# Kernel tuning notes

Hardware: AMD Instinct MI355X
Metric: run time of the kernel (lower is better)

## Reference

```python
import jax, jax.numpy as jnp
import numpy as np

NEG_INF = -1.0e9


def setup_inputs() -> dict:
    key = jax.random.key(0)
    k1, k2, k3, k4 = jax.random.split(key, 4)
    B, N, F, U, H = 4, 2048, 128, 64, 4
    x = jax.random.normal(k1, (B, N, F), dtype=jnp.float32)
    adj = jax.random.randint(k2, (B, N, N), 0, 2, dtype=jnp.int32)
    W = jax.random.normal(k3, (H, F, U), dtype=jnp.float32) * (1.0 / np.sqrt(F))
    b = jnp.zeros((H, U), dtype=jnp.float32)
    a_w = jax.random.normal(k4, (H, U), dtype=jnp.float32) * (1.0 / np.sqrt(U))
    a_b = jnp.zeros((H,), dtype=jnp.float32)
    return {"x": x, "adj": adj, "W": W, "b": b, "a_w": a_w, "a_b": a_b}


def reference(x, adj, W, b, a_w, a_b):
    # Per-head Dense + relu, batched over heads: proj [H,B,N,U]
    proj = jax.nn.relu(jnp.einsum('bnf,hfu->hbnu', x, W) + b[:, None, None, :])
    # Scalar attention score per node: s [H,B,N]
    s = jnp.einsum('hbnu,hu->hbn', proj, a_w) + a_b[:, None, None]
    # Outer-product logits [H,B,N,N], masked by adjacency
    logits = s[:, :, :, None] * s[:, :, None, :]
    logits = jnp.where(adj[None] > 0, logits, NEG_INF)
    scores = jax.nn.softmax(logits, axis=-1)
    # Weighted aggregation, then mean over heads -> [B,N,U]
    out = jnp.einsum('hbij,hbju->hbiu', scores, proj)
    return jnp.mean(out, axis=0)
```

## Files before the change

### kernel.cpp

```cpp
#include <hip/hip_runtime.h>
#include <hip/hip_bf16.h>


#define Bdim 4
#define Ndim 2048
#define Fdim 128
#define Udim 64
#define Hdim 4
#define JC 2
#define JCHUNK (Ndim / JC)

typedef __attribute__((ext_vector_type(8))) short short8;
typedef __attribute__((ext_vector_type(4))) float f32x4;

__device__ __forceinline__ void splitbf(float f, short& hi, short& lo) {
  union { __hip_bfloat16 b; unsigned short u; } ch, cl;
  ch.b = __float2bfloat16(f);
  cl.b = __float2bfloat16(f - __bfloat162float(ch.b));
  hi = (short)ch.u;
  lo = (short)cl.u;
}

__device__ __forceinline__ void stage16(const void* g, void* l) {
  __builtin_amdgcn_global_load_lds(
      (const __attribute__((address_space(1))) unsigned int*)g,
      (__attribute__((address_space(3))) unsigned int*)l, 16, 0, 0);
}

__global__ __launch_bounds__(256) void pack_adj_kernel(
    const int* __restrict__ adj, unsigned long long* __restrict__ bits,
    int nchunks) {
  const int lane = threadIdx.x & 63;
  const int wid = (blockIdx.x * 256 + threadIdx.x) >> 6;
  const int nw = (gridDim.x * 256) >> 6;
  for (int c = wid * 4; c + 3 < nchunks; c += nw * 4) {
    int v0 = adj[(size_t)(c + 0) * 64 + lane];
    int v1 = adj[(size_t)(c + 1) * 64 + lane];
    int v2 = adj[(size_t)(c + 2) * 64 + lane];
    int v3 = adj[(size_t)(c + 3) * 64 + lane];
    unsigned long long m0 = __ballot(v0 != 0);
    unsigned long long m1 = __ballot(v1 != 0);
    unsigned long long m2 = __ballot(v2 != 0);
    unsigned long long m3 = __ballot(v3 != 0);
    if (lane == 0) {
      bits[c + 0] = m0;
      bits[c + 1] = m1;
      bits[c + 2] = m2;
      bits[c + 3] = m3;
    }
  }
}

__global__ __launch_bounds__(256) void proj_kernel(
    const float* __restrict__ x, const float* __restrict__ W,
    const float* __restrict__ bias, const float* __restrict__ a_w,
    const float* __restrict__ a_b, unsigned short* __restrict__ pTh,
    unsigned short* __restrict__ pTl, float* __restrict__ s) {
  const int bid = blockIdx.x;
  const int nt = bid & 31;
  const int b = (bid >> 5) & 3;
  const int h = bid >> 7;
  const int n0 = nt * 64;

  __shared__ __align__(16) char smem[71168];
  float (*Wl)[Udim] = (float(*)[Udim])(smem);
  float (*xl)[Fdim + 4] = (float(*)[Fdim + 4])(smem + 32768);
  float (*pt)[68] = (float(*)[68])(smem + 32768);
  float* bl = (float*)(smem + 66560);
  float* awl = (float*)(smem + 66816);
  float (*sred)[16] = (float(*)[16])(smem + 67072);

  const int t = threadIdx.x;

  const float* Wg = W + (size_t)h * Fdim * Udim;
  for (int k = t; k < Fdim * Udim / 4; k += 256) {
    ((float4*)&Wl[0][0])[k] = ((const float4*)Wg)[k];
  }
  if (t < Udim) {
    bl[t] = bias[h * Udim + t];
    awl[t] = a_w[h * Udim + t];
  }
  const float* xg = x + ((size_t)b * Ndim + n0) * Fdim;
  for (int k = t; k < 64 * Fdim / 4; k += 256) {
    int row = k >> 5;
    int c4 = k & 31;
    float4 v = ((const float4*)xg)[(size_t)row * (Fdim / 4) + c4];
    *(float4*)&xl[row][c4 * 4] = v;
  }
  __syncthreads();

  const int ug = t & 15, rg = t >> 4;
  const int u0 = ug * 4, r0 = rg * 4;
  float acc[4][4] = {};

#pragma unroll 4
  for (int f = 0; f < Fdim; ++f) {
    const float4 wv = *(const float4*)&Wl[f][u0];
    const float xv[4] = {xl[r0][f], xl[r0 + 1][f], xl[r0 + 2][f], xl[r0 + 3][f]};
#pragma unroll
    for (int c = 0; c < 4; ++c) {
      acc[c][0] = fmaf(xv[c], wv.x, acc[c][0]);
      acc[c][1] = fmaf(xv[c], wv.y, acc[c][1]);
      acc[c][2] = fmaf(xv[c], wv.z, acc[c][2]);
      acc[c][3] = fmaf(xv[c], wv.w, acc[c][3]);
    }
  }

  float po[4][4];
#pragma unroll
  for (int c = 0; c < 4; ++c)
#pragma unroll
    for (int k = 0; k < 4; ++k)
      po[c][k] = fmaxf(acc[c][k] + bl[u0 + k], 0.f);

#pragma unroll
  for (int c = 0; c < 4; ++c) {
    float sp = po[c][0] * awl[u0 + 0] + po[c][1] * awl[u0 + 1] +
               po[c][2] * awl[u0 + 2] + po[c][3] * awl[u0 + 3];
    sred[r0 + c][ug] = sp;
  }
  __syncthreads();

#pragma unroll
  for (int k = 0; k < 4; ++k) {
    float4 v = {po[0][k], po[1][k], po[2][k], po[3][k]};
    *(float4*)&pt[u0 + k][r0] = v;
  }
  __syncthreads();

  const size_t hb = (size_t)h * Bdim + b;
  const int su = t >> 2;
  const int snl = (t & 3) * 16;
  float v[16];
#pragma unroll
  for (int j = 0; j < 4; ++j)
    *(float4*)&v[4 * j] = *(const float4*)&pt[su][snl + 4 * j];
  short hi[16], lo[16];
#pragma unroll
  for (int k = 0; k < 16; ++k) splitbf(v[k], hi[k], lo[k]);
  unsigned short* ph =
      pTh + hb * (size_t)(Udim * Ndim) + (size_t)su * Ndim + n0 + snl;
  unsigned short* pl =
      pTl + hb * (size_t)(Udim * Ndim) + (size_t)su * Ndim + n0 + snl;
  *(short8*)(ph + 0) = *(short8*)&hi[0];
  *(short8*)(ph + 8) = *(short8*)&hi[8];
  *(short8*)(pl + 0) = *(short8*)&lo[0];
  *(short8*)(pl + 8) = *(short8*)&lo[8];

  if (t < 64) {
    float sum = a_b[h];
#pragma unroll
    for (int k = 0; k < 16; ++k) sum += sred[t][k];
    s[hb * Ndim + n0 + t] = sum;
  }
}

__global__ __launch_bounds__(256, 4) void attn_mfma_kernel(
    const unsigned short* __restrict__ pTh,
    const unsigned short* __restrict__ pTl, const float* __restrict__ s,
    const unsigned int* __restrict__ abits, float* __restrict__ out_part,
    float* __restrict__ Z_part) {
  const int bid = blockIdx.x;
  const int jc = bid & 1;
  const int it = (bid >> 1) & 31;
  const int b = (bid >> 6) & 3;
  const int h = bid >> 8;
  const int i0g = it * 64;
  const int j0g = jc * JCHUNK;

  __shared__ float sj[JCHUNK];
  __shared__ unsigned int ab[64][33];
  __shared__ short Bst[2][8][512];
  __shared__ float zl[4][4][16];

  const int t = threadIdx.x;
  const int wv = t >> 6;
  const int lane = t & 63;
  const int q = lane >> 4;
  const int li = lane & 15;
  const size_t hb = (size_t)h * Bdim + b;
  const float* sg = s + hb * Ndim;

  ((float4*)sj)[t] = ((const float4*)(sg + j0g))[t];
  for (int k = t; k < 64 * 32; k += 256) {
    int row = k >> 5, w = k & 31;
    ab[row][w] =
        abits[((size_t)b * Ndim + i0g + row) * (Ndim / 32) + (j0g >> 5) + w];
  }
  const int irow = wv * 16 + li;

  const unsigned short* bsrc_h =
      pTh + hb * (size_t)(Udim * Ndim) + (size_t)(wv * 16 + li) * Ndim + j0g +
      q * 8;
  const unsigned short* bsrc_l =
      pTl + hb * (size_t)(Udim * Ndim) + (size_t)(wv * 16 + li) * Ndim + j0g +
      q * 8;

  stage16(bsrc_h, &Bst[0][wv * 2 + 0][0]);
  stage16(bsrc_l, &Bst[0][wv * 2 + 1][0]);

  f32x4 acc[4] = {};
  float zacc = 0.f;
  __syncthreads();

  const float si = sg[i0g + irow];
  int buf = 0;

  for (int js = 0; js < JCHUNK; js += 32) {
    if (js + 32 < JCHUNK) {
      stage16(bsrc_h + js + 32, &Bst[buf ^ 1][wv * 2 + 0][0]);
      stage16(bsrc_l + js + 32, &Bst[buf ^ 1][wv * 2 + 1][0]);
    }
    const short8 b0h = *(const short8*)&Bst[buf][0][lane * 8];
    const short8 b0l = *(const short8*)&Bst[buf][1][lane * 8];
    const short8 b1h = *(const short8*)&Bst[buf][2][lane * 8];
    const short8 b1l = *(const short8*)&Bst[buf][3][lane * 8];
    const short8 b2h = *(const short8*)&Bst[buf][4][lane * 8];
    const short8 b2l = *(const short8*)&Bst[buf][5][lane * 8];
    const short8 b3h = *(const short8*)&Bst[buf][6][lane * 8];
    const short8 b3l = *(const short8*)&Bst[buf][7][lane * 8];
    const unsigned int mb = (ab[irow][js >> 5] >> (q * 8)) & 0xffu;
    const f32x4 s0 = *(const f32x4*)&sj[js + q * 8];
    const f32x4 s1 = *(const f32x4*)&sj[js + q * 8 + 4];
    const float sv[8] = {s0.x, s0.y, s0.z, s0.w, s1.x, s1.y, s1.z, s1.w};
    short8 ahi, alo;
#pragma unroll
    for (int e = 0; e < 8; ++e) {
      float we = __expf(si * sv[e]);
      we = ((mb >> e) & 1u) ? we : 0.f;
      zacc += we;
      short hh, ll;
      splitbf(we, hh, ll);
      ahi[e] = hh;
      alo[e] = ll;
    }
    acc[0] = __builtin_amdgcn_mfma_f32_16x16x32_bf16(ahi, b0h, acc[0], 0, 0, 0);
    acc[1] = __builtin_amdgcn_mfma_f32_16x16x32_bf16(ahi, b1h, acc[1], 0, 0, 0);
    acc[2] = __builtin_amdgcn_mfma_f32_16x16x32_bf16(ahi, b2h, acc[2], 0, 0, 0);
    acc[3] = __builtin_amdgcn_mfma_f32_16x16x32_bf16(ahi, b3h, acc[3], 0, 0, 0);
    acc[0] = __builtin_amdgcn_mfma_f32_16x16x32_bf16(alo, b0h, acc[0], 0, 0, 0);
    acc[1] = __builtin_amdgcn_mfma_f32_16x16x32_bf16(alo, b1h, acc[1], 0, 0, 0);
    acc[2] = __builtin_amdgcn_mfma_f32_16x16x32_bf16(alo, b2h, acc[2], 0, 0, 0);
    acc[3] = __builtin_amdgcn_mfma_f32_16x16x32_bf16(alo, b3h, acc[3], 0, 0, 0);
    acc[0] = __builtin_amdgcn_mfma_f32_16x16x32_bf16(ahi, b0l, acc[0], 0, 0, 0);
    acc[1] = __builtin_amdgcn_mfma_f32_16x16x32_bf16(ahi, b1l, acc[1], 0, 0, 0);
    acc[2] = __builtin_amdgcn_mfma_f32_16x16x32_bf16(ahi, b2l, acc[2], 0, 0, 0);
    acc[3] = __builtin_amdgcn_mfma_f32_16x16x32_bf16(ahi, b3l, acc[3], 0, 0, 0);
    __syncthreads();
    buf ^= 1;
  }

  zl[wv][q][li] = zacc;
  __syncthreads();

  const size_t pslab = ((size_t)h * JC + jc) * Bdim + b;
  if (q == 0) {
    float z = zl[wv][0][li] + zl[wv][1][li] + zl[wv][2][li] + zl[wv][3][li];
    Z_part[pslab * Ndim + i0g + wv * 16 + li] = z;
  }
  float* op = out_part + (pslab * Ndim + i0g + wv * 16) * Udim;
#pragma unroll
  for (int r = 0; r < 4; ++r) {
    const int ir = q * 4 + r;
#pragma unroll
    for (int m = 0; m < 4; ++m) {
      op[(size_t)ir * Udim + m * 16 + li] = acc[m][r];
    }
  }
}

__global__ __launch_bounds__(256) void combine_kernel(
    const float* __restrict__ out_part, const float* __restrict__ Z_part,
    float* __restrict__ out) {
  const int idx = blockIdx.x * 256 + threadIdx.x;
  const int u4 = idx & 15;
  const size_t bn = (size_t)(idx >> 4);
  float4 r = {0.f, 0.f, 0.f, 0.f};
#pragma unroll
  for (int h = 0; h < Hdim; ++h) {
    const size_t s0 = ((size_t)h * JC + 0) * (Bdim * Ndim) + bn;
    const size_t s1 = ((size_t)h * JC + 1) * (Bdim * Ndim) + bn;
    float4 p0 = ((const float4*)out_part)[s0 * (Udim / 4) + u4];
    float4 p1 = ((const float4*)out_part)[s1 * (Udim / 4) + u4];
    float z = Z_part[s0] + Z_part[s1];
    z = (z != 0.f) ? z : 1.f;
    const float inv = 1.f / z;
    r.x += (p0.x + p1.x) * inv;
    r.y += (p0.y + p1.y) * inv;
    r.z += (p0.z + p1.z) * inv;
    r.w += (p0.w + p1.w) * inv;
  }
  r.x *= 0.25f; r.y *= 0.25f; r.z *= 0.25f; r.w *= 0.25f;
  ((float4*)out)[idx] = r;
}

extern "C" void kernel_launch(void* const* d_in, const int* in_sizes, int n_in,
                              void* d_out, int out_size, void* d_ws,
                              size_t ws_size, hipStream_t stream) {
  const float* x = (const float*)d_in[0];
  const int* adj = (const int*)d_in[1];
  const float* W = (const float*)d_in[2];
  const float* bias = (const float*)d_in[3];
  const float* a_w = (const float*)d_in[4];
  const float* a_b = (const float*)d_in[5];
  float* out = (float*)d_out;

  char* ws = (char*)d_ws;
  unsigned short* pTh = (unsigned short*)(ws + 0);
  unsigned short* pTl = (unsigned short*)(ws + 4194304);
  float* s = (float*)(ws + 8388608);
  unsigned int* adjbits = (unsigned int*)(ws + 8519680);
  float* out_part = (float*)(ws + 10616832);
  float* Z_part = (float*)(ws + 27394048);

  const int nchunks = Bdim * Ndim * Ndim / 64;
  pack_adj_kernel<<<2048, 256, 0, stream>>>(adj, (unsigned long long*)adjbits,
                                            nchunks);
  proj_kernel<<<Hdim * Bdim * 32, 256, 0, stream>>>(x, W, bias, a_w, a_b, pTh,
                                                    pTl, s);
  attn_mfma_kernel<<<Hdim * Bdim * 32 * JC, 256, 0, stream>>>(
      pTh, pTl, s, adjbits, out_part, Z_part);
  combine_kernel<<<(Bdim * Ndim * Udim / 4) / 256, 256, 0, stream>>>(
      out_part, Z_part, out);
}
```

Before: 166.4 us.

## Split attention over four j-chunks, stage output through LDS, shuffle-reduce Z

Doubles the number of j-column chunks per attention block, so there are twice as many blocks, each with half the work and a smaller shared-memory footprint, and raises the occupancy hint to 7 blocks. The Z partial sums are now reduced with wave shuffles instead of LDS, and accumulator output goes through a transposed LDS buffer so global stores are float4 and coalesced. The hi/lo bf16 split now truncates for the high part. The costs are more partial-output traffic and a combine kernel that sums four chunks instead of two.

```diff
diff --git a/kernel.cpp b/kernel.cpp
--- a/kernel.cpp
+++ b/kernel.cpp
@@ -7,18 +7,23 @@
 #define Fdim 128
 #define Udim 64
 #define Hdim 4
-#define JC 2
+#define JC 4
 #define JCHUNK (Ndim / JC)
 
 typedef __attribute__((ext_vector_type(8))) short short8;
 typedef __attribute__((ext_vector_type(4))) float f32x4;
 
+__device__ __forceinline__ short bf16_rne(float f) {
+  union { __hip_bfloat16 b; unsigned short u; } c;
+  c.b = __float2bfloat16(f);
+  return (short)c.u;
+}
+
 __device__ __forceinline__ void splitbf(float f, short& hi, short& lo) {
-  union { __hip_bfloat16 b; unsigned short u; } ch, cl;
-  ch.b = __float2bfloat16(f);
-  cl.b = __float2bfloat16(f - __bfloat162float(ch.b));
-  hi = (short)ch.u;
-  lo = (short)cl.u;
+  unsigned u = __float_as_uint(f);
+  hi = (short)(u >> 16);
+  float lof = f - __uint_as_float(u & 0xffff0000u);
+  lo = bf16_rne(lof);
 }
 
 __device__ __forceinline__ void stage16(const void* g, void* l) {
@@ -155,23 +160,22 @@
   }
 }
 
-__global__ __launch_bounds__(256, 4) void attn_mfma_kernel(
+__global__ __launch_bounds__(256, 7) void attn_mfma_kernel(
     const unsigned short* __restrict__ pTh,
     const unsigned short* __restrict__ pTl, const float* __restrict__ s,
     const unsigned int* __restrict__ abits, float* __restrict__ out_part,
     float* __restrict__ Z_part) {
   const int bid = blockIdx.x;
-  const int jc = bid & 1;
-  const int it = (bid >> 1) & 31;
-  const int b = (bid >> 6) & 3;
-  const int h = bid >> 8;
+  const int jc = bid & 3;
+  const int it = (bid >> 2) & 31;
+  const int b = (bid >> 7) & 3;
+  const int h = bid >> 9;
   const int i0g = it * 64;
   const int j0g = jc * JCHUNK;
 
   __shared__ float sj[JCHUNK];
-  __shared__ unsigned int ab[64][33];
-  __shared__ short Bst[2][8][512];
-  __shared__ float zl[4][4][16];
+  __shared__ unsigned int ab[64][16];
+  __shared__ __align__(16) short Bst[2][8][512];
 
   const int t = threadIdx.x;
   const int wv = t >> 6;
@@ -181,11 +185,12 @@
   const size_t hb = (size_t)h * Bdim + b;
   const float* sg = s + hb * Ndim;
 
-  ((float4*)sj)[t] = ((const float4*)(sg + j0g))[t];
-  for (int k = t; k < 64 * 32; k += 256) {
-    int row = k >> 5, w = k & 31;
-    ab[row][w] =
-        abits[((size_t)b * Ndim + i0g + row) * (Ndim / 32) + (j0g >> 5) + w];
+  ((float2*)sj)[t] = ((const float2*)(sg + j0g))[t];
+  {
+    const int row = t >> 2, w4 = (t & 3) * 4;
+    *(uint4*)&ab[row][w4] = *(const uint4*)&abits[((size_t)b * Ndim + i0g +
+                                                   row) * (Ndim / 32) +
+                                                  (j0g >> 5) + w4];
   }
   const int irow = wv * 16 + li;
 
@@ -250,22 +255,26 @@
     buf ^= 1;
   }
 
-  zl[wv][q][li] = zacc;
-  __syncthreads();
-
+  zacc += __shfl_xor(zacc, 16, 64);
+  zacc += __shfl_xor(zacc, 32, 64);
   const size_t pslab = ((size_t)h * JC + jc) * Bdim + b;
-  if (q == 0) {
-    float z = zl[wv][0][li] + zl[wv][1][li] + zl[wv][2][li] + zl[wv][3][li];
-    Z_part[pslab * Ndim + i0g + wv * 16 + li] = z;
-  }
-  float* op = out_part + (pslab * Ndim + i0g + wv * 16) * Udim;
-#pragma unroll
-  for (int r = 0; r < 4; ++r) {
-    const int ir = q * 4 + r;
-#pragma unroll
-    for (int m = 0; m < 4; ++m) {
-      op[(size_t)ir * Udim + m * 16 + li] = acc[m][r];
-    }
+  if (q == 0) Z_part[pslab * Ndim + i0g + wv * 16 + li] = zacc;
+
+  float* cbuf = (float*)&Bst[0][0][0];
+#pragma unroll
+  for (int r = 0; r < 4; ++r)
+#pragma unroll
+    for (int m = 0; m < 4; ++m)
+      cbuf[wv * 1024 + (q * 4 + r) * 64 + m * 16 + li] = acc[m][r];
+  __syncthreads();
+  {
+    const int row = lane >> 2, c0 = (lane & 3) * 16;
+    const float* src = &cbuf[wv * 1024 + row * 64 + c0];
+    float* op =
+        out_part + (pslab * Ndim + i0g + wv * 16 + row) * Udim + c0;
+#pragma unroll
+    for (int k = 0; k < 4; ++k)
+      *(float4*)(op + k * 4) = *(const float4*)(src + k * 4);
   }
 }
 
@@ -278,17 +287,21 @@
   float4 r = {0.f, 0.f, 0.f, 0.f};
 #pragma unroll
   for (int h = 0; h < Hdim; ++h) {
-    const size_t s0 = ((size_t)h * JC + 0) * (Bdim * Ndim) + bn;
-    const size_t s1 = ((size_t)h * JC + 1) * (Bdim * Ndim) + bn;
-    float4 p0 = ((const float4*)out_part)[s0 * (Udim / 4) + u4];
-    float4 p1 = ((const float4*)out_part)[s1 * (Udim / 4) + u4];
-    float z = Z_part[s0] + Z_part[s1];
+    float4 p = {0.f, 0.f, 0.f, 0.f};
+    float z = 0.f;
+#pragma unroll
+    for (int j = 0; j < JC; ++j) {
+      const size_t sl = ((size_t)h * JC + j) * (Bdim * Ndim) + bn;
+      float4 pj = ((const float4*)out_part)[sl * (Udim / 4) + u4];
+      p.x += pj.x; p.y += pj.y; p.z += pj.z; p.w += pj.w;
+      z += Z_part[sl];
+    }
     z = (z != 0.f) ? z : 1.f;
     const float inv = 1.f / z;
-    r.x += (p0.x + p1.x) * inv;
-    r.y += (p0.y + p1.y) * inv;
-    r.z += (p0.z + p1.z) * inv;
-    r.w += (p0.w + p1.w) * inv;
+    r.x += p.x * inv;
+    r.y += p.y * inv;
+    r.z += p.z * inv;
+    r.w += p.w * inv;
   }
   r.x *= 0.25f; r.y *= 0.25f; r.z *= 0.25f; r.w *= 0.25f;
   ((float4*)out)[idx] = r;
@@ -311,7 +324,7 @@
   float* s = (float*)(ws + 8388608);
   unsigned int* adjbits = (unsigned int*)(ws + 8519680);
   float* out_part = (float*)(ws + 10616832);
-  float* Z_part = (float*)(ws + 27394048);
+  float* Z_part = (float*)(ws + 44171264);
 
   const int nchunks = Bdim * Ndim * Ndim / 64;
   pack_adj_kernel<<<2048, 256, 0, stream>>>(adj, (unsigned long long*)adjbits,
```

Result: slower. 171.4 us (+3.0%).
